# Kernel tuning notes

Hardware: AMD Instinct MI355X
Metric: run time of the kernel (lower is better)

Reference implementation:

```python
import jax, jax.numpy as jnp
import numpy as np

B, T, C = 2, 2048, 2048
NH, NKV, D = 16, 4, 128
N_REP = NH // NKV
THETA = 10000.0


def setup_inputs() -> dict:
    key = jax.random.key(0)
    ks = jax.random.split(key, 5)
    s = 0.02
    return {
        "x": jax.random.normal(ks[0], (B, T, C), dtype=jnp.float32),
        "Wq": jax.random.normal(ks[1], (C, C), dtype=jnp.float32) * s,
        "Wk": jax.random.normal(ks[2], (NKV * D, C), dtype=jnp.float32) * s,
        "Wv": jax.random.normal(ks[3], (NKV * D, C), dtype=jnp.float32) * s,
        "Wo": jax.random.normal(ks[4], (C, C), dtype=jnp.float32) * s,
    }


def _rope(t):
    # t: (B, H, T, D); rotate pairs (even, odd) by angle pos * theta_i
    inv_freq = 1.0 / (THETA ** (jnp.arange(0, D, 2, dtype=jnp.float32) / D))  # (D/2,)
    ang = jnp.arange(T, dtype=jnp.float32)[:, None] * inv_freq[None, :]       # (T, D/2)
    cos, sin = jnp.cos(ang), jnp.sin(ang)
    te, to = t[..., 0::2], t[..., 1::2]
    re = te * cos - to * sin
    ro = te * sin + to * cos
    return jnp.stack([re, ro], axis=-1).reshape(t.shape).astype(t.dtype)


def reference(x, Wq, Wk, Wv, Wo):
    # Projections (Linear: y = x @ W.T)
    q = (x @ Wq.T).reshape(B, T, NH, D).transpose(0, 2, 1, 3)    # (B,NH,T,D)
    k = (x @ Wk.T).reshape(B, T, NKV, D).transpose(0, 2, 1, 3)   # (B,NKV,T,D)
    v = (x @ Wv.T).reshape(B, T, NKV, D).transpose(0, 2, 1, 3)
    q = _rope(q)
    k = _rope(k)
    # GQA: group query heads per kv head instead of materializing repeated K/V
    qg = q.reshape(B, NKV, N_REP, T, D)                          # (B,G,R,T,D)
    scale = 1.0 / jnp.sqrt(jnp.float32(D))
    scores = jnp.einsum("bgrtd,bgsd->bgrts", qg, k) * scale      # (B,G,R,T,T)
    causal = jnp.tril(jnp.ones((T, T), dtype=bool))
    scores = jnp.where(causal, scores, jnp.finfo(scores.dtype).min)
    attn = jax.nn.softmax(scores, axis=-1)
    out = jnp.einsum("bgrts,bgsd->bgrtd", attn, v)               # (B,G,R,T,D)
    out = out.reshape(B, NH, T, D).transpose(0, 2, 1, 3).reshape(B, T, C)
    return out @ Wo.T
```

## Files before the change

### kernel.cpp

```cpp
#include <hip/hip_runtime.h>
#include <hip/hip_bf16.h>
#include <stdint.h>

#define B_   2
#define T_   2048
#define C_   2048
#define NH_  16
#define NKV_ 4
#define D_   128
#define NREP_ 4

typedef __attribute__((ext_vector_type(8))) short bf16x8;
typedef __attribute__((ext_vector_type(4))) float f32x4;

__device__ inline short f2bs(float f) {
    __hip_bfloat16 h = __float2bfloat16(f);
    return *reinterpret_cast<short*>(&h);
}
__device__ inline float bs2f(unsigned short s) {
    __hip_bfloat16 h = *reinterpret_cast<__hip_bfloat16*>(&s);
    return __bfloat162float(h);
}

__device__ inline void gl_lds16(const __hip_bfloat16* g, __hip_bfloat16* l) {
    __builtin_amdgcn_global_load_lds(
        (const __attribute__((address_space(1))) unsigned int*)g,
        (__attribute__((address_space(3))) unsigned int*)l,
        16, 0, 0);
}

__global__ void cvt_f32_bf16(const float* __restrict__ src,
                             __hip_bfloat16* __restrict__ dst, int n) {
    int i = (blockIdx.x * blockDim.x + threadIdx.x) * 4;
    if (i >= n) return;
    float4 v = *reinterpret_cast<const float4*>(src + i);
    short4 o;
    o.x = f2bs(v.x); o.y = f2bs(v.y); o.z = f2bs(v.z); o.w = f2bs(v.w);
    *reinterpret_cast<short4*>(dst + i) = o;
}

__device__ inline void storeC(float* p, float v) { *p = v; }
__device__ inline void storeC(__hip_bfloat16* p, float v) { *p = __float2bfloat16(v); }

template <typename OutT>
__global__ __launch_bounds__(256) void gemm_bt(const __hip_bfloat16* __restrict__ A,
                                               const __hip_bfloat16* __restrict__ Bm,
                                               OutT* __restrict__ Cm,
                                               int M, int N, int K) {
    __shared__ __hip_bfloat16 As[128 * 32];
    __shared__ __hip_bfloat16 Bs[128 * 32];
    const int tid  = threadIdx.x;
    const int lane = tid & 63;
    const int wv   = tid >> 6;
    const int m0 = blockIdx.y * 128, n0 = blockIdx.x * 128;
    const int wm = (wv >> 1) * 64, wn = (wv & 1) * 64;
    const int q16 = lane >> 4, r16 = lane & 15;

    f32x4 acc[4][4] = {};

    const int lrow = tid >> 2;
    const int lcol = (tid & 3) * 8;
    const __hip_bfloat16* aG = A  + (size_t)(m0 + lrow) * K + lcol;
    const __hip_bfloat16* bG = Bm + (size_t)(n0 + lrow) * K + lcol;
    __hip_bfloat16* aL = As + tid * 8;
    __hip_bfloat16* bL = Bs + tid * 8;

    for (int k0 = 0; k0 < K; k0 += 32) {
        __syncthreads();
        gl_lds16(aG + k0,          aL);
        gl_lds16(aG + 64 * K + k0, aL + 2048);
        gl_lds16(bG + k0,          bL);
        gl_lds16(bG + 64 * K + k0, bL + 2048);
        __syncthreads();
        bf16x8 af[4], bfr[4];
#pragma unroll
        for (int i = 0; i < 4; i++)
            af[i] = *reinterpret_cast<const bf16x8*>(As + (wm + i * 16 + r16) * 32 + q16 * 8);
#pragma unroll
        for (int j = 0; j < 4; j++)
            bfr[j] = *reinterpret_cast<const bf16x8*>(Bs + (wn + j * 16 + r16) * 32 + q16 * 8);
#pragma unroll
        for (int i = 0; i < 4; i++)
#pragma unroll
            for (int j = 0; j < 4; j++)
                acc[i][j] = __builtin_amdgcn_mfma_f32_16x16x32_bf16(af[i], bfr[j], acc[i][j], 0, 0, 0);
    }

#pragma unroll
    for (int i = 0; i < 4; i++)
#pragma unroll
        for (int j = 0; j < 4; j++)
#pragma unroll
            for (int r = 0; r < 4; r++) {
                int row = m0 + wm + i * 16 + q16 * 4 + r;
                int col = n0 + wn + j * 16 + r16;
                storeC(&Cm[(size_t)row * N + col], acc[i][j][r]);
            }
}

__global__ void rope_scatter(const __hip_bfloat16* __restrict__ y,
                             __hip_bfloat16* __restrict__ qo,
                             __hip_bfloat16* __restrict__ ko,
                             __hip_bfloat16* __restrict__ vT) {
    int idx = blockIdx.x * blockDim.x + threadIdx.x;
    if (idx >= (B_ * T_) * 1536) return;
    int m = idx / 1536, pc = idx % 1536;
    int b = m / T_, t = m % T_;
    int n = pc * 2;
    ushort2 uv = *reinterpret_cast<const ushort2*>(y + (size_t)m * 3072 + n);
    float e = bs2f(uv.x), od = bs2f(uv.y);

    if (n < 2560) {
        int nn = (n < 2048) ? n : (n - 2048);
        int dloc = nn & 127;
        int p = dloc >> 1;
        float inv = __expf(-(float)p * (9.210340371976184f / 64.0f));
        float ang = (float)t * inv;
        float c = cosf(ang), s = sinf(ang);
        float re = e * c - od * s;
        float ro = e * s + od * c;
        ushort2 w;
        w.x = (unsigned short)f2bs(re);
        w.y = (unsigned short)f2bs(ro);
        if (n < 2048) {
            int h = n >> 7;
            *reinterpret_cast<ushort2*>(qo + ((size_t)(b * NH_ + h) * T_ + t) * D_ + dloc) = w;
        } else {
            int h = nn >> 7;
            *reinterpret_cast<ushort2*>(ko + ((size_t)(b * NKV_ + h) * T_ + t) * D_ + dloc) = w;
        }
    } else {
        int nn = n - 2560;
        int h = nn >> 7, d = nn & 127;
        __hip_bfloat16* base = vT + (size_t)(b * NKV_ + h) * D_ * T_;
        base[(size_t)d * T_ + t]       = __float2bfloat16(e);
        base[(size_t)(d + 1) * T_ + t] = __float2bfloat16(od);
    }
}

__global__ __launch_bounds__(256, 3) void attn_kernel(const __hip_bfloat16* __restrict__ Q,
                                                      const __hip_bfloat16* __restrict__ Kt,
                                                      const __hip_bfloat16* __restrict__ Vt,
                                                      __hip_bfloat16* __restrict__ Ao) {
    __shared__ __hip_bfloat16 Ks[2][4096];
    __shared__ __hip_bfloat16 Vs[2][4096];
    __shared__ __hip_bfloat16 Pl[4][1280];

    const int lane = threadIdx.x & 63, wv = threadIdx.x >> 6;
    const int bg = blockIdx.y;
    const int tb = (int)(gridDim.x - 1) - (int)blockIdx.x;
    const int b = bg >> 2, g = bg & 3;
    const int h = g * 4 + wv;
    const int t0 = tb * 32;
    const int q16 = lane >> 4, r16 = lane & 15;

    const __hip_bfloat16* qh = Q + ((size_t)((b * NH_ + h) * T_) + t0) * D_;
    const __hip_bfloat16* kh = Kt + (size_t)(b * NKV_ + g) * T_ * D_;
    const __hip_bfloat16* vh = Vt + (size_t)(b * NKV_ + g) * D_ * T_;

    bf16x8 bqA[4], bqB[4];
#pragma unroll
    for (int kk = 0; kk < 4; kk++) {
        bqA[kk] = *reinterpret_cast<const bf16x8*>(qh + (size_t)r16 * D_ + kk * 32 + q16 * 8);
        bqB[kk] = *reinterpret_cast<const bf16x8*>(qh + (size_t)(16 + r16) * D_ + kk * 32 + q16 * 8);
    }

    float liA = 0.f, liB = 0.f;
    f32x4 oA[8], oB[8];
#pragma unroll
    for (int d = 0; d < 8; d++) {
        oA[d] = (f32x4){0.f, 0.f, 0.f, 0.f};
        oB[d] = (f32x4){0.f, 0.f, 0.f, 0.f};
    }

    const float SCL2 = 0.088388347648318447f * 1.4426950408889634f;
    const int tqA = t0 + r16;
    const int tqB = t0 + 16 + r16;
    const int nIter = tb + 1;

    const __hip_bfloat16* gK = kh + (size_t)((wv & 1) * 16 + r16) * D_ + q16 * 8;
    const __hip_bfloat16* gV = vh + (size_t)(((wv - 2) * 4) * 16 + r16) * T_ + q16 * 8;

#define STAGE(bufi, s0_)                                                        \
    do {                                                                        \
        if (wv < 2) {                                                           \
            const __hip_bfloat16* gp = gK + (size_t)(s0_) * D_;                 \
            __hip_bfloat16* lp = &Ks[bufi][(wv * 4) * 512] + lane * 8;          \
            gl_lds16(gp,      lp);                                              \
            gl_lds16(gp + 32, lp + 512);                                        \
            gl_lds16(gp + 64, lp + 1024);                                       \
            gl_lds16(gp + 96, lp + 1536);                                       \
        } else {                                                                \
            const __hip_bfloat16* gp = gV + (s0_);                              \
            __hip_bfloat16* lp = &Vs[bufi][((wv - 2) * 4) * 512] + lane * 8;    \
            gl_lds16(gp,                      lp);                              \
            gl_lds16(gp + (size_t)16 * T_,    lp + 512);                        \
            gl_lds16(gp + (size_t)32 * T_,    lp + 1024);                       \
            gl_lds16(gp + (size_t)48 * T_,    lp + 1536);                       \
        }                                                                       \
    } while (0)

    STAGE(0, 0);

    for (int it = 0; it < nIter; it++) {
        const int s0 = it * 32;
        const int cur = it & 1;
        __syncthreads();
        if (it + 1 < nIter) STAGE(cur ^ 1, s0 + 32);

        f32x4 sc0A = (f32x4){0.f, 0.f, 0.f, 0.f};
        f32x4 sc1A = (f32x4){0.f, 0.f, 0.f, 0.f};
        f32x4 sc0B = (f32x4){0.f, 0.f, 0.f, 0.f};
        f32x4 sc1B = (f32x4){0.f, 0.f, 0.f, 0.f};
        {
            bf16x8 ak[4];
#pragma unroll
            for (int kk = 0; kk < 4; kk++)
                ak[kk] = *reinterpret_cast<const bf16x8*>(&Ks[cur][kk * 512] + lane * 8);
#pragma unroll
            for (int kk = 0; kk < 4; kk++) {
                sc0A = __builtin_amdgcn_mfma_f32_16x16x32_bf16(ak[kk], bqA[kk], sc0A, 0, 0, 0);
                sc0B = __builtin_amdgcn_mfma_f32_16x16x32_bf16(ak[kk], bqB[kk], sc0B, 0, 0, 0);
            }
#pragma unroll
            for (int kk = 0; kk < 4; kk++)
                ak[kk] = *reinterpret_cast<const bf16x8*>(&Ks[cur][(4 + kk) * 512] + lane * 8);
#pragma unroll
            for (int kk = 0; kk < 4; kk++) {
                sc1A = __builtin_amdgcn_mfma_f32_16x16x32_bf16(ak[kk], bqA[kk], sc1A, 0, 0, 0);
                sc1B = __builtin_amdgcn_mfma_f32_16x16x32_bf16(ak[kk], bqB[kk], sc1B, 0, 0, 0);
            }
        }

        ushort4 w0A, w1A, w0B, w1B;
        float psA = 0.f, psB = 0.f;
#pragma unroll
        for (int r = 0; r < 4; r++) {
            int s_a = s0 + q16 * 4 + r;
            float pa0 = (s_a <= tqA)      ? __builtin_amdgcn_exp2f(sc0A[r] * SCL2) : 0.f;
            float pa1 = (s_a + 16 <= tqA) ? __builtin_amdgcn_exp2f(sc1A[r] * SCL2) : 0.f;
            float pb0 = (s_a <= tqB)      ? __builtin_amdgcn_exp2f(sc0B[r] * SCL2) : 0.f;
            float pb1 = (s_a + 16 <= tqB) ? __builtin_amdgcn_exp2f(sc1B[r] * SCL2) : 0.f;
            psA += pa0 + pa1;
            psB += pb0 + pb1;
            ((unsigned short*)&w0A)[r] = (unsigned short)f2bs(pa0);
            ((unsigned short*)&w1A)[r] = (unsigned short)f2bs(pa1);
            ((unsigned short*)&w0B)[r] = (unsigned short)f2bs(pb0);
            ((unsigned short*)&w1B)[r] = (unsigned short)f2bs(pb1);
        }
        liA += psA;
        liB += psB;

        *reinterpret_cast<ushort4*>(&Pl[wv][r16 * 40 + q16 * 4]) = w0A;
        *reinterpret_cast<ushort4*>(&Pl[wv][r16 * 40 + 16 + q16 * 4]) = w1A;
        *reinterpret_cast<ushort4*>(&Pl[wv][640 + r16 * 40 + q16 * 4]) = w0B;
        *reinterpret_cast<ushort4*>(&Pl[wv][640 + r16 * 40 + 16 + q16 * 4]) = w1B;
        asm volatile("s_waitcnt lgkmcnt(0)" ::: "memory");
        bf16x8 pfA = *reinterpret_cast<const bf16x8*>(&Pl[wv][r16 * 40 + q16 * 8]);
        bf16x8 pfB = *reinterpret_cast<const bf16x8*>(&Pl[wv][640 + r16 * 40 + q16 * 8]);

#pragma unroll
        for (int d = 0; d < 8; d++) {
            bf16x8 bv = *reinterpret_cast<const bf16x8*>(&Vs[cur][d * 512] + lane * 8);
            oA[d] = __builtin_amdgcn_mfma_f32_16x16x32_bf16(pfA, bv, oA[d], 0, 0, 0);
            oB[d] = __builtin_amdgcn_mfma_f32_16x16x32_bf16(pfB, bv, oB[d], 0, 0, 0);
        }
    }

    liA += __shfl_xor(liA, 16);
    liA += __shfl_xor(liA, 32);
    liB += __shfl_xor(liB, 16);
    liB += __shfl_xor(liB, 32);
#pragma unroll
    for (int r = 0; r < 4; r++) {
        float lrA = __shfl(liA, q16 * 4 + r, 16);
        float lrB = __shfl(liB, q16 * 4 + r, 16);
        float invA = 1.0f / lrA;
        float invB = 1.0f / lrB;
        int tA = t0 + q16 * 4 + r;
        __hip_bfloat16* dstA = Ao + (size_t)(b * T_ + tA) * C_ + h * D_ + r16;
        __hip_bfloat16* dstB = dstA + (size_t)16 * C_;
#pragma unroll
        for (int d = 0; d < 8; d++) {
            dstA[d * 16] = __float2bfloat16(oA[d][r] * invA);
            dstB[d * 16] = __float2bfloat16(oB[d][r] * invB);
        }
    }
#undef STAGE
}

extern "C" void kernel_launch(void* const* d_in, const int* in_sizes, int n_in,
                              void* d_out, int out_size, void* d_ws, size_t ws_size,
                              hipStream_t stream) {
    const float* x  = (const float*)d_in[0];
    const float* Wq = (const float*)d_in[1];
    const float* Wk = (const float*)d_in[2];
    const float* Wv = (const float*)d_in[3];
    const float* Wo = (const float*)d_in[4];
    float* out = (float*)d_out;
    char* ws = (char*)d_ws;

    __hip_bfloat16* xb   = (__hip_bfloat16*)(ws + 0);
    __hip_bfloat16* wcat = (__hip_bfloat16*)(ws + 16777216);
    __hip_bfloat16* wob  = (__hip_bfloat16*)(ws + 29360128);
    __hip_bfloat16* yq   = (__hip_bfloat16*)(ws + 37748736);
    __hip_bfloat16* qatt = (__hip_bfloat16*)(ws + 62914560);
    __hip_bfloat16* katt = (__hip_bfloat16*)(ws + 79691776);
    __hip_bfloat16* vT   = (__hip_bfloat16*)(ws + 83886080);
    __hip_bfloat16* aout = (__hip_bfloat16*)(ws + 88080384);

    const int thr = 256;
    cvt_f32_bf16<<<(B_ * T_ * C_ / 4 + thr - 1) / thr, thr, 0, stream>>>(x, xb, B_ * T_ * C_);
    cvt_f32_bf16<<<(C_ * C_ / 4 + thr - 1) / thr, thr, 0, stream>>>(Wq, wcat, C_ * C_);
    cvt_f32_bf16<<<(512 * 2048 / 4 + thr - 1) / thr, thr, 0, stream>>>(Wk, wcat + C_ * C_, 512 * 2048);
    cvt_f32_bf16<<<(512 * 2048 / 4 + thr - 1) / thr, thr, 0, stream>>>(Wv, wcat + C_ * C_ + 512 * 2048, 512 * 2048);
    cvt_f32_bf16<<<(C_ * C_ / 4 + thr - 1) / thr, thr, 0, stream>>>(Wo, wob, C_ * C_);

    gemm_bt<__hip_bfloat16><<<dim3(24, 32), 256, 0, stream>>>(xb, wcat, yq, 4096, 3072, 2048);

    rope_scatter<<<(B_ * T_ * 1536 + thr - 1) / thr, thr, 0, stream>>>(yq, qatt, katt, vT);

    attn_kernel<<<dim3(64, 8), 256, 0, stream>>>(qatt, katt, vT, aout);

    gemm_bt<float><<<dim3(16, 32), 256, 0, stream>>>(aout, wob, out, 4096, 2048, 2048);
}
```

Baseline: 342.7 us.

## Split attention KV range across two blocks and combine partials

Each query tile's causal KV loop is split into two halves run by separate blocks, so the grid doubles to 128x8 and long tiles no longer dominate the tail. Partial unnormalized outputs and row sums go to workspace, and a new combine kernel sums them and normalizes. The P-matrix reshuffle through LDS is replaced by cross-lane shuffles, and occupancy hint rises to 4 blocks. This adds an extra kernel launch, extra global traffic for bf16 partials, and a bf16 rounding of partials before summation. It relies on the softmax having no running max, which the code before already assumed.

Measured after the change: 501.6 us. +46.4%, slower.

```diff
diff --git a/kernel.cpp b/kernel.cpp
--- a/kernel.cpp
+++ b/kernel.cpp
@@ -138,22 +138,48 @@
     }
 }
 
-__global__ __launch_bounds__(256, 3) void attn_kernel(const __hip_bfloat16* __restrict__ Q,
+__device__ inline bf16x8 pf_gather(const ushort4& w0, const ushort4& w1,
+                                   int q16, int r16) {
+    int2 a0 = *reinterpret_cast<const int2*>(&w0);
+    int2 a1 = *reinterpret_cast<const int2*>(&w1);
+    int srcLo = ((q16 & 1) << 5) + r16;
+    int srcHi = srcLo + 16;
+    int lo0x = __shfl(a0.x, srcLo), lo0y = __shfl(a0.y, srcLo);
+    int lo1x = __shfl(a1.x, srcLo), lo1y = __shfl(a1.y, srcLo);
+    int hi0x = __shfl(a0.x, srcHi), hi0y = __shfl(a0.y, srcHi);
+    int hi1x = __shfl(a1.x, srcHi), hi1y = __shfl(a1.y, srcHi);
+    bool lw = (q16 < 2);
+    int4 pk;
+    pk.x = lw ? lo0x : lo1x;
+    pk.y = lw ? lo0y : lo1y;
+    pk.z = lw ? hi0x : hi1x;
+    pk.w = lw ? hi0y : hi1y;
+    return *reinterpret_cast<bf16x8*>(&pk);
+}
+
+__global__ __launch_bounds__(256, 4) void attn_kernel(const __hip_bfloat16* __restrict__ Q,
                                                       const __hip_bfloat16* __restrict__ Kt,
                                                       const __hip_bfloat16* __restrict__ Vt,
-                                                      __hip_bfloat16* __restrict__ Ao) {
+                                                      __hip_bfloat16* __restrict__ Op0,
+                                                      __hip_bfloat16* __restrict__ Op1,
+                                                      float* __restrict__ LiP) {
     __shared__ __hip_bfloat16 Ks[2][4096];
     __shared__ __hip_bfloat16 Vs[2][4096];
-    __shared__ __hip_bfloat16 Pl[4][1280];
 
     const int lane = threadIdx.x & 63, wv = threadIdx.x >> 6;
     const int bg = blockIdx.y;
-    const int tb = (int)(gridDim.x - 1) - (int)blockIdx.x;
+    const int xr = 127 - (int)blockIdx.x;
+    const int tb = xr >> 1, half = xr & 1;
     const int b = bg >> 2, g = bg & 3;
     const int h = g * 4 + wv;
     const int t0 = tb * 32;
     const int q16 = lane >> 4, r16 = lane & 15;
 
+    const int n    = tb + 1;
+    const int nlo  = (n + 1) >> 1;
+    const int it0   = half ? nlo : 0;
+    const int itEnd = half ? n   : nlo;
+
     const __hip_bfloat16* qh = Q + ((size_t)((b * NH_ + h) * T_) + t0) * D_;
     const __hip_bfloat16* kh = Kt + (size_t)(b * NKV_ + g) * T_ * D_;
     const __hip_bfloat16* vh = Vt + (size_t)(b * NKV_ + g) * D_ * T_;
@@ -176,7 +202,6 @@
     const float SCL2 = 0.088388347648318447f * 1.4426950408889634f;
     const int tqA = t0 + r16;
     const int tqB = t0 + 16 + r16;
-    const int nIter = tb + 1;
 
     const __hip_bfloat16* gK = kh + (size_t)((wv & 1) * 16 + r16) * D_ + q16 * 8;
     const __hip_bfloat16* gV = vh + (size_t)(((wv - 2) * 4) * 16 + r16) * T_ + q16 * 8;
@@ -200,13 +225,13 @@
         }                                                                       \
     } while (0)
 
-    STAGE(0, 0);
-
-    for (int it = 0; it < nIter; it++) {
+    if (it0 < itEnd) STAGE(it0 & 1, it0 * 32);
+
+    for (int it = it0; it < itEnd; it++) {
         const int s0 = it * 32;
         const int cur = it & 1;
         __syncthreads();
-        if (it + 1 < nIter) STAGE(cur ^ 1, s0 + 32);
+        if (it + 1 < itEnd) STAGE(cur ^ 1, (it + 1) * 32);
 
         f32x4 sc0A = (f32x4){0.f, 0.f, 0.f, 0.f};
         f32x4 sc1A = (f32x4){0.f, 0.f, 0.f, 0.f};
@@ -251,13 +276,8 @@
         liA += psA;
         liB += psB;
 
-        *reinterpret_cast<ushort4*>(&Pl[wv][r16 * 40 + q16 * 4]) = w0A;
-        *reinterpret_cast<ushort4*>(&Pl[wv][r16 * 40 + 16 + q16 * 4]) = w1A;
-        *reinterpret_cast<ushort4*>(&Pl[wv][640 + r16 * 40 + q16 * 4]) = w0B;
-        *reinterpret_cast<ushort4*>(&Pl[wv][640 + r16 * 40 + 16 + q16 * 4]) = w1B;
-        asm volatile("s_waitcnt lgkmcnt(0)" ::: "memory");
-        bf16x8 pfA = *reinterpret_cast<const bf16x8*>(&Pl[wv][r16 * 40 + q16 * 8]);
-        bf16x8 pfB = *reinterpret_cast<const bf16x8*>(&Pl[wv][640 + r16 * 40 + q16 * 8]);
+        bf16x8 pfA = pf_gather(w0A, w1A, q16, r16);
+        bf16x8 pfB = pf_gather(w0B, w1B, q16, r16);
 
 #pragma unroll
         for (int d = 0; d < 8; d++) {
@@ -271,22 +291,52 @@
     liA += __shfl_xor(liA, 32);
     liB += __shfl_xor(liB, 16);
     liB += __shfl_xor(liB, 32);
+
+    const int tile = bg * 64 + tb;
+    __hip_bfloat16* od = (half ? Op1 : Op0) + ((size_t)(tile * 4 + wv)) * 4096;
 #pragma unroll
     for (int r = 0; r < 4; r++) {
-        float lrA = __shfl(liA, q16 * 4 + r, 16);
-        float lrB = __shfl(liB, q16 * 4 + r, 16);
-        float invA = 1.0f / lrA;
-        float invB = 1.0f / lrB;
-        int tA = t0 + q16 * 4 + r;
-        __hip_bfloat16* dstA = Ao + (size_t)(b * T_ + tA) * C_ + h * D_ + r16;
-        __hip_bfloat16* dstB = dstA + (size_t)16 * C_;
+        int qA = q16 * 4 + r;
 #pragma unroll
         for (int d = 0; d < 8; d++) {
-            dstA[d * 16] = __float2bfloat16(oA[d][r] * invA);
-            dstB[d * 16] = __float2bfloat16(oB[d][r] * invB);
-        }
-    }
+            od[qA * 128 + d * 16 + r16]        = __float2bfloat16(oA[d][r]);
+            od[(qA + 16) * 128 + d * 16 + r16] = __float2bfloat16(oB[d][r]);
+        }
+    }
+    float* lp = LiP + ((size_t)(tile * 2 + half)) * 128 + wv * 32;
+    if (q16 == 0) lp[r16] = liA;
+    if (q16 == 1) lp[16 + r16] = liB;
 #undef STAGE
+}
+
+__global__ void attn_combine(const __hip_bfloat16* __restrict__ O0,
+                             const __hip_bfloat16* __restrict__ O1,
+                             const float* __restrict__ Li,
+                             __hip_bfloat16* __restrict__ Ao) {
+    int idx = blockIdx.x * blockDim.x + threadIdx.x;
+    int dv   = idx & 15;
+    int q    = (idx >> 4) & 31;
+    int hw   = (idx >> 9) & 3;
+    int tile = idx >> 11;
+    int bg = tile >> 6, tb = tile & 63;
+    int b = bg >> 2, g = bg & 3;
+
+    size_t obase = ((size_t)(tile * 4 + hw)) * 4096 + q * 128 + dv * 8;
+    bf16x8 v0 = *reinterpret_cast<const bf16x8*>(O0 + obase);
+    bf16x8 v1 = *reinterpret_cast<const bf16x8*>(O1 + obase);
+    float li = Li[(size_t)(tile * 2) * 128 + hw * 32 + q] +
+               Li[(size_t)(tile * 2 + 1) * 128 + hw * 32 + q];
+    float inv = 1.0f / li;
+
+    int t = tb * 32 + q;
+    int h = g * 4 + hw;
+    bf16x8 ov;
+#pragma unroll
+    for (int j = 0; j < 8; j++) {
+        float s = bs2f(((const unsigned short*)&v0)[j]) + bs2f(((const unsigned short*)&v1)[j]);
+        ov[j] = f2bs(s * inv);
+    }
+    *reinterpret_cast<bf16x8*>(Ao + ((size_t)(b * T_ + t)) * C_ + h * D_ + dv * 8) = ov;
 }
 
 extern "C" void kernel_launch(void* const* d_in, const int* in_sizes, int n_in,
@@ -309,6 +359,10 @@
     __hip_bfloat16* vT   = (__hip_bfloat16*)(ws + 83886080);
     __hip_bfloat16* aout = (__hip_bfloat16*)(ws + 88080384);
 
+    __hip_bfloat16* Op0 = (__hip_bfloat16*)(ws + 0);
+    __hip_bfloat16* Op1 = (__hip_bfloat16*)(ws + 37748736);
+    float*          LiP = (float*)(ws + 54525952);
+
     const int thr = 256;
     cvt_f32_bf16<<<(B_ * T_ * C_ / 4 + thr - 1) / thr, thr, 0, stream>>>(x, xb, B_ * T_ * C_);
     cvt_f32_bf16<<<(C_ * C_ / 4 + thr - 1) / thr, thr, 0, stream>>>(Wq, wcat, C_ * C_);
@@ -320,7 +374,8 @@
 
     rope_scatter<<<(B_ * T_ * 1536 + thr - 1) / thr, thr, 0, stream>>>(yq, qatt, katt, vT);
 
-    attn_kernel<<<dim3(64, 8), 256, 0, stream>>>(qatt, katt, vT, aout);
+    attn_kernel<<<dim3(128, 8), 256, 0, stream>>>(qatt, katt, vT, Op0, Op1, LiP);
+    attn_combine<<<4096, 256, 0, stream>>>(Op0, Op1, LiP, aout);
 
     gemm_bt<float><<<dim3(16, 32), 256, 0, stream>>>(aout, wob, out, 4096, 2048, 2048);
 }
```
